# Optimization experiments

Measured on AMD Instinct MI355X. Metric: run time of the kernel, lower is better.

The kernel has to match this reference:

```python
import jax, jax.numpy as jnp
import numpy as np

D = 768
H = 12
DH = D // H
DFF = 4 * D
B, S = 2, 2048


def setup_inputs() -> dict:
    key = jax.random.key(0)
    ks = jax.random.split(key, 12)
    inp = {
        "X": jax.random.normal(ks[0], (B, S, D), dtype=jnp.float32),
        # per-head projections, stacked over heads (nn.Linear: y = x W^T + b; we store W already transposed as [d, d_h])
        "Wq": jax.random.normal(ks[1], (H, D, DH), dtype=jnp.float32) * (1.0 / np.sqrt(D)),
        "bq": jnp.zeros((H, DH), dtype=jnp.float32),
        "Wk": jax.random.normal(ks[2], (H, D, DH), dtype=jnp.float32) * (1.0 / np.sqrt(D)),
        "bk": jnp.zeros((H, DH), dtype=jnp.float32),
        "Wv": jax.random.normal(ks[3], (H, D, DH), dtype=jnp.float32) * (1.0 / np.sqrt(D)),
        "bv": jnp.zeros((H, DH), dtype=jnp.float32),
        "W0": jax.random.normal(ks[4], (D, D), dtype=jnp.float32) * (1.0 / np.sqrt(D)),
        "b0": jnp.zeros((D,), dtype=jnp.float32),
        # FFN params are torch.randn (unit std) in the original
        "W1": jax.random.normal(ks[5], (D, DFF), dtype=jnp.float32),
        "b1": jnp.zeros((DFF,), dtype=jnp.float32),
        "W2": jax.random.normal(ks[6], (DFF, D), dtype=jnp.float32),
        "b2": jnp.zeros((D,), dtype=jnp.float32),
        "g1": jnp.ones((D,), dtype=jnp.float32),
        "o1": jnp.zeros((D,), dtype=jnp.float32),
        "g2": jnp.ones((D,), dtype=jnp.float32),
        "o2": jnp.zeros((D,), dtype=jnp.float32),
    }
    return inp


def _layernorm(x, gain, offset):
    # original: (x - mean) / (std + 1e-5)  with population std (unbiased=False)
    m = jnp.mean(x, axis=-1, keepdims=True)
    sd = jnp.sqrt(jnp.mean((x - m) ** 2, axis=-1, keepdims=True))
    return gain * ((x - m) / (sd + 1e-5)) + offset


def _mha(x, Wq, bq, Wk, bk, Wv, bv, W0, b0):
    # batched over heads; equivalent to the per-head SHA loop + concat
    q = jnp.einsum("bsd,hdk->bhsk", x, Wq) + bq[None, :, None, :]
    k = jnp.einsum("bsd,hdk->bhsk", x, Wk) + bk[None, :, None, :]
    v = jnp.einsum("bsd,hdk->bhsk", x, Wv) + bv[None, :, None, :]
    scores = jnp.einsum("bhsk,bhtk->bhst", q, k) / np.sqrt(DH).astype(np.float32)
    seq = x.shape[1]
    causal = jnp.tril(jnp.ones((seq, seq), dtype=bool))
    scores = jnp.where(causal[None, None], scores, -jnp.inf)
    w = jax.nn.softmax(scores, axis=-1)
    out = jnp.einsum("bhst,bhtk->bhsk", w, v)
    out = jnp.transpose(out, (0, 2, 1, 3)).reshape(x.shape[0], seq, D)  # concat heads
    return out @ W0 + b0


def reference(X, Wq, bq, Wk, bk, Wv, bv, W0, b0, W1, b1, W2, b2, g1, o1, g2, o2):
    h = X + _mha(_layernorm(X, g1, o1), Wq, bq, Wk, bk, Wv, bv, W0, b0)
    y = _layernorm(h, g2, o2)
    y = jnp.maximum(y @ W1 + b1, 0.0) @ W2 + b2
    return h + y
```

## Files before the change

kernel.cpp:

```cpp
#include <hip/hip_runtime.h>
#include <hip/hip_bf16.h>
#include <cstdint>

#define BB 2
#define SS 2048
#define DD 768
#define HH 12
#define DHH 64
#define DFF 3072
#define MM (BB * SS)

typedef __attribute__((ext_vector_type(8))) short bf16x8;
typedef __attribute__((ext_vector_type(4))) float f32x4;
typedef __attribute__((ext_vector_type(16))) float f32x16;
typedef __attribute__((ext_vector_type(4))) unsigned short u16x4;
typedef __attribute__((ext_vector_type(8))) unsigned short u16x8;
typedef unsigned int u32;

#define DEV static __device__ __forceinline__

typedef __attribute__((address_space(1))) void AS1void;
typedef __attribute__((address_space(3))) void AS3void;

DEV void async_copy16(const void* g, void* l) {
  __builtin_amdgcn_global_load_lds((AS1void*)g, (AS3void*)l, 16, 0, 0);
}

DEV unsigned short bf16bits(float f) {
  __hip_bfloat16 h = __float2bfloat16(f);
  return *(unsigned short*)&h;
}

DEV u32 pack2(float a, float b) {
  return ((u32)bf16bits(b) << 16) | (u32)bf16bits(a);
}

__global__ __launch_bounds__(256) void ln_kernel(
    const float* __restrict__ x, const float* __restrict__ gain,
    const float* __restrict__ off, __hip_bfloat16* __restrict__ out)
{
  const int wave = threadIdx.x >> 6;
  const int lane = threadIdx.x & 63;
  const int row = blockIdx.x * 4 + wave;
  const float* xr = x + (size_t)row * DD;

  float4 v[3];
  float s1 = 0.f, s2 = 0.f;
#pragma unroll
  for (int j = 0; j < 3; ++j) {
    v[j] = *(const float4*)(xr + (j * 64 + lane) * 4);
    s1 += v[j].x + v[j].y + v[j].z + v[j].w;
    s2 += v[j].x * v[j].x + v[j].y * v[j].y + v[j].z * v[j].z + v[j].w * v[j].w;
  }
#pragma unroll
  for (int d = 1; d < 64; d <<= 1) {
    s1 += __shfl_xor(s1, d);
    s2 += __shfl_xor(s2, d);
  }
  const float mean = s1 * (1.0f / 768.0f);
  const float var = fmaxf(s2 * (1.0f / 768.0f) - mean * mean, 0.0f);
  const float rs = 1.0f / (sqrtf(var) + 1e-5f);

  unsigned short* orow = (unsigned short*)out + (size_t)row * DD;
#pragma unroll
  for (int j = 0; j < 3; ++j) {
    const int c = (j * 64 + lane) * 4;
    float4 g4 = *(const float4*)(gain + c);
    float4 o4 = *(const float4*)(off + c);
    u16x4 pk;
    pk[0] = bf16bits(g4.x * ((v[j].x - mean) * rs) + o4.x);
    pk[1] = bf16bits(g4.y * ((v[j].y - mean) * rs) + o4.y);
    pk[2] = bf16bits(g4.z * ((v[j].z - mean) * rs) + o4.z);
    pk[3] = bf16bits(g4.w * ((v[j].w - mean) * rs) + o4.w);
    *(u16x4*)(orow + c) = pk;
  }
}

__global__ __launch_bounds__(256) void transpose_generic(
    const float* __restrict__ in, __hip_bfloat16* __restrict__ out, int R, int C)
{
  __shared__ float tile[64][65];
  const int c0 = blockIdx.x * 64, r0 = blockIdx.y * 64;
  for (int i = threadIdx.x; i < 4096; i += 256) {
    int r = i >> 6, c = i & 63;
    tile[r][c] = in[(size_t)(r0 + r) * C + c0 + c];
  }
  __syncthreads();
  for (int i = threadIdx.x; i < 4096; i += 256) {
    int c = i >> 6, r = i & 63;
    out[(size_t)(c0 + c) * R + r0 + r] = __float2bfloat16(tile[r][c]);
  }
}

__global__ __launch_bounds__(256) void transpose_qkv(
    const float* __restrict__ Wq, const float* __restrict__ Wk,
    const float* __restrict__ Wv, __hip_bfloat16* __restrict__ out)
{
  __shared__ float tile[64][65];
  const int z = blockIdx.z;
  const int p = z / HH, h = z - p * HH;
  const float* in = (p == 0 ? Wq : (p == 1 ? Wk : Wv)) + (size_t)h * DD * DHH;
  const int r0 = blockIdx.y * 64;
  for (int i = threadIdx.x; i < 4096; i += 256) {
    int r = i >> 6, c = i & 63;
    tile[r][c] = in[(size_t)(r0 + r) * DHH + c];
  }
  __syncthreads();
  for (int i = threadIdx.x; i < 4096; i += 256) {
    int c = i >> 6, r = i & 63;
    out[(size_t)(p * DD + h * DHH + c) * DD + r0 + r] = __float2bfloat16(tile[r][c]);
  }
}

__global__ __launch_bounds__(256) void kvimg_kernel(
    const __hip_bfloat16* __restrict__ qkv, char* __restrict__ kimg,
    char* __restrict__ vimg)
{
  __shared__ unsigned short tileK[64][72];
  __shared__ unsigned short tileV[64][72];
  const int bh = blockIdx.y;
  const int b = bh / HH, h = bh - (bh / HH) * HH;
  const int t0 = blockIdx.x * 64;
  const int HD = 3 * DD;
  const unsigned short* Kp = (const unsigned short*)qkv + (size_t)(b * SS) * HD + DD + h * DHH;
  const unsigned short* Vp = (const unsigned short*)qkv + (size_t)(b * SS) * HD + 2 * DD + h * DHH;
  char* kdst = kimg + ((size_t)bh * 32 + blockIdx.x) * 8192;
  char* vdst = vimg + ((size_t)bh * 32 + blockIdx.x) * 8192;

  for (int i = threadIdx.x; i < 512; i += 256) {
    const int r = i >> 3, c8 = (i & 7) * 8;
    *(bf16x8*)&tileK[r][c8] = *(const bf16x8*)(Kp + (size_t)(t0 + r) * HD + c8);
    *(bf16x8*)&tileV[r][c8] = *(const bf16x8*)(Vp + (size_t)(t0 + r) * HD + c8);
  }
  __syncthreads();
  for (int i = threadIdx.x; i < 512; i += 256) {
    const int f = i >> 6, l = i & 63;
    const int kc = f >> 1, half = f & 1;
    const int lc = l & 31, lh = l >> 5;
    *(bf16x8*)(kdst + i * 16) = *(const bf16x8*)&tileK[half * 32 + lc][kc * 16 + lh * 8];
    union { unsigned short u[8]; bf16x8 v; } w;
#pragma unroll
    for (int e = 0; e < 8; ++e) w.u[e] = tileV[kc * 16 + lh * 8 + e][half * 32 + lc];
    *(bf16x8*)(vdst + i * 16) = w.v;
  }
}

template<bool RELU, bool OUT_BF16, bool HAS_RES>
__global__ __launch_bounds__(256) void gemm_bt(
    const __hip_bfloat16* __restrict__ A, const __hip_bfloat16* __restrict__ BT,
    const float* __restrict__ bias, const float* __restrict__ res,
    void* __restrict__ outp, int M, int N, int K)
{
  __shared__ __hip_bfloat16 Alds[2][128 * 32];
  __shared__ __hip_bfloat16 Blds[2][128 * 32];
  const int tid = threadIdx.x;
  const int wave = tid >> 6;
  const int lane = tid & 63;
  const int fr = lane & 15, fq = lane >> 4;
  const int wr = wave >> 1, wc = wave & 1;
  const int bm = blockIdx.y * 128, bn = blockIdx.x * 128;

  const int srow = tid >> 2;
  const int scol = (tid & 3) * 8;
  const __hip_bfloat16* ag0 = A + (size_t)(bm + srow) * K + scol;
  const __hip_bfloat16* ag1 = A + (size_t)(bm + 64 + srow) * K + scol;
  const __hip_bfloat16* bg0 = BT + (size_t)(bn + srow) * K + scol;
  const __hip_bfloat16* bg1 = BT + (size_t)(bn + 64 + srow) * K + scol;
  const int so = wave * 512;

  f32x4 acc[4][4] = {};

  async_copy16(ag0, &Alds[0][so]);
  async_copy16(ag1, &Alds[0][2048 + so]);
  async_copy16(bg0, &Blds[0][so]);
  async_copy16(bg1, &Blds[0][2048 + so]);
  __syncthreads();

  const int niter = K / 32;
  for (int i = 0; i < niter; ++i) {
    const int cur = i & 1;
    if (i + 1 < niter) {
      const int k1 = (i + 1) * 32;
      async_copy16(ag0 + k1, &Alds[cur ^ 1][so]);
      async_copy16(ag1 + k1, &Alds[cur ^ 1][2048 + so]);
      async_copy16(bg0 + k1, &Blds[cur ^ 1][so]);
      async_copy16(bg1 + k1, &Blds[cur ^ 1][2048 + so]);
    }
    bf16x8 af[4], bfr[4];
#pragma unroll
    for (int i4 = 0; i4 < 4; ++i4)
      af[i4] = *(const bf16x8*)(&Alds[cur][(wr * 64 + i4 * 16 + fr) * 32 + fq * 8]);
#pragma unroll
    for (int j4 = 0; j4 < 4; ++j4)
      bfr[j4] = *(const bf16x8*)(&Blds[cur][(wc * 64 + j4 * 16 + fr) * 32 + fq * 8]);
#pragma unroll
    for (int i4 = 0; i4 < 4; ++i4)
#pragma unroll
      for (int j4 = 0; j4 < 4; ++j4)
        acc[i4][j4] = __builtin_amdgcn_mfma_f32_16x16x32_bf16(af[i4], bfr[j4], acc[i4][j4], 0, 0, 0);
    __syncthreads();
  }

#pragma unroll
  for (int j = 0; j < 4; ++j) {
    const int c = bn + wc * 64 + j * 16 + fr;
    const float bv = bias[c];
#pragma unroll
    for (int i = 0; i < 4; ++i) {
#pragma unroll
      for (int r = 0; r < 4; ++r) {
        const int rr = bm + wr * 64 + i * 16 + fq * 4 + r;
        float v = acc[i][j][r] + bv;
        if (RELU) v = fmaxf(v, 0.0f);
        if (HAS_RES) v += res[(size_t)rr * N + c];
        if (OUT_BF16) ((__hip_bfloat16*)outp)[(size_t)rr * N + c] = __float2bfloat16(v);
        else          ((float*)outp)[(size_t)rr * N + c] = v;
      }
    }
  }
}

__global__ __launch_bounds__(256) void gemm_bt_sk(
    const __hip_bfloat16* __restrict__ A, const __hip_bfloat16* __restrict__ BT,
    float* __restrict__ part01, float* __restrict__ part23,
    int M, int N, int K, int K_per)
{
  __shared__ __hip_bfloat16 Alds[2][128 * 32];
  __shared__ __hip_bfloat16 Blds[2][128 * 32];
  const int tid = threadIdx.x;
  const int wave = tid >> 6;
  const int lane = tid & 63;
  const int fr = lane & 15, fq = lane >> 4;
  const int wr = wave >> 1, wc = wave & 1;
  const int bm = blockIdx.y * 128, bn = blockIdx.x * 128;
  const int z = blockIdx.z;
  float* part = (z < 2 ? part01 : part23) + (size_t)(z & 1) * M * N;
  const int kbase = z * K_per;

  const int srow = tid >> 2;
  const int scol = (tid & 3) * 8;
  const __hip_bfloat16* ag0 = A + (size_t)(bm + srow) * K + scol + kbase;
  const __hip_bfloat16* ag1 = A + (size_t)(bm + 64 + srow) * K + scol + kbase;
  const __hip_bfloat16* bg0 = BT + (size_t)(bn + srow) * K + scol + kbase;
  const __hip_bfloat16* bg1 = BT + (size_t)(bn + 64 + srow) * K + scol + kbase;
  const int so = wave * 512;

  f32x4 acc[4][4] = {};

  async_copy16(ag0, &Alds[0][so]);
  async_copy16(ag1, &Alds[0][2048 + so]);
  async_copy16(bg0, &Blds[0][so]);
  async_copy16(bg1, &Blds[0][2048 + so]);
  __syncthreads();

  const int niter = K_per / 32;
  for (int i = 0; i < niter; ++i) {
    const int cur = i & 1;
    if (i + 1 < niter) {
      const int k1 = (i + 1) * 32;
      async_copy16(ag0 + k1, &Alds[cur ^ 1][so]);
      async_copy16(ag1 + k1, &Alds[cur ^ 1][2048 + so]);
      async_copy16(bg0 + k1, &Blds[cur ^ 1][so]);
      async_copy16(bg1 + k1, &Blds[cur ^ 1][2048 + so]);
    }
    bf16x8 af[4], bfr[4];
#pragma unroll
    for (int i4 = 0; i4 < 4; ++i4)
      af[i4] = *(const bf16x8*)(&Alds[cur][(wr * 64 + i4 * 16 + fr) * 32 + fq * 8]);
#pragma unroll
    for (int j4 = 0; j4 < 4; ++j4)
      bfr[j4] = *(const bf16x8*)(&Blds[cur][(wc * 64 + j4 * 16 + fr) * 32 + fq * 8]);
#pragma unroll
    for (int i4 = 0; i4 < 4; ++i4)
#pragma unroll
      for (int j4 = 0; j4 < 4; ++j4)
        acc[i4][j4] = __builtin_amdgcn_mfma_f32_16x16x32_bf16(af[i4], bfr[j4], acc[i4][j4], 0, 0, 0);
    __syncthreads();
  }

#pragma unroll
  for (int j = 0; j < 4; ++j) {
    const int c = bn + wc * 64 + j * 16 + fr;
#pragma unroll
    for (int i = 0; i < 4; ++i) {
#pragma unroll
      for (int r = 0; r < 4; ++r) {
        const int rr = bm + wr * 64 + i * 16 + fq * 4 + r;
        part[(size_t)rr * N + c] = acc[i][j][r];
      }
    }
  }
}

__global__ __launch_bounds__(256) void combine4(
    const float* __restrict__ part01, const float* __restrict__ part23,
    const float* __restrict__ res, const float* __restrict__ bias,
    float* __restrict__ out, int MN, int N)
{
  const int idx = (blockIdx.x * 256 + threadIdx.x) * 4;
  if (idx >= MN) return;
  const float4 a0 = *(const float4*)(part01 + idx);
  const float4 a1 = *(const float4*)(part01 + MN + idx);
  const float4 a2 = *(const float4*)(part23 + idx);
  const float4 a3 = *(const float4*)(part23 + MN + idx);
  const float4 rr = *(const float4*)(res + idx);
  const float4 bb = *(const float4*)(bias + (idx % N));
  float4 o;
  o.x = a0.x + a1.x + a2.x + a3.x + rr.x + bb.x;
  o.y = a0.y + a1.y + a2.y + a3.y + rr.y + bb.y;
  o.z = a0.z + a1.z + a2.z + a3.z + rr.z + bb.z;
  o.w = a0.w + a1.w + a2.w + a3.w + rr.w + bb.w;
  *(float4*)(out + idx) = o;
}

__global__ __launch_bounds__(128, 3) void attn_kernel(
    const __hip_bfloat16* __restrict__ qkv, const char* __restrict__ kimg,
    const char* __restrict__ vimg, __hip_bfloat16* __restrict__ outp)
{
  const int HD = 3 * DD;
  const int id = blockIdx.x;
  const int xcd = id & 7;
  const int j = id >> 3;
  const int s2 = 63 - j / 3;
  const int bhl = j - 3 * (j / 3);
  const int bh = xcd * 3 + bhl;
  const int b = bh / HH, h = bh - (bh / HH) * HH;

  const int q0w = s2 * 32;
  const int tid = threadIdx.x;
  const int c = tid >> 6;
  const int lane = tid & 63;
  const int col = lane & 31, hi = lane >> 5;
  const int qg = q0w + col;

  const size_t base = (size_t)b * SS * HD;
  const __hip_bfloat16* Qp = qkv + base + h * DHH;
  const char* kimg_h = kimg + (size_t)bh * 32 * 8192;
  const char* vimg_h = vimg + (size_t)bh * 32 * 8192;

  __shared__ __align__(16) char sm[17408];

  bf16x8 qf[4];
#pragma unroll
  for (int kc = 0; kc < 4; ++kc)
    qf[kc] = *(const bf16x8*)(Qp + (size_t)qg * HD + kc * 16 + hi * 8);

  f32x16 o0 = {}, o1 = {};
  float mreg = -1e30f, lreg = 0.f;
  const float CS = 0.125f * 1.44269504f;

  const int ntiles = (q0w >> 6) + 1;

  bf16x8 kf[8];
  {
    const char* ks = kimg_h + (size_t)c * 8192 + lane * 16;
#pragma unroll
    for (int f = 0; f < 8; ++f) kf[f] = *(const bf16x8*)(ks + f * 1024);
  }

  for (int t = c; t < ntiles; t += 2) {
    const int kv0 = t * 64;
    f32x16 s0 = {}, s1 = {};
    __builtin_amdgcn_s_setprio(1);
#pragma unroll
    for (int kc = 0; kc < 4; ++kc) {
      s0 = __builtin_amdgcn_mfma_f32_32x32x16_bf16(kf[kc * 2],     qf[kc], s0, 0, 0, 0);
      s1 = __builtin_amdgcn_mfma_f32_32x32x16_bf16(kf[kc * 2 + 1], qf[kc], s1, 0, 0, 0);
    }
    __builtin_amdgcn_s_setprio(0);
    bf16x8 vf[8];
    {
      const char* vs = vimg_h + (size_t)t * 8192 + lane * 16;
#pragma unroll
      for (int f = 0; f < 8; ++f) vf[f] = *(const bf16x8*)(vs + f * 1024);
    }
    if (t + 2 < ntiles) {
      const char* ks = kimg_h + (size_t)(t + 2) * 8192 + lane * 16;
#pragma unroll
      for (int f = 0; f < 8; ++f) kf[f] = *(const bf16x8*)(ks + f * 1024);
    }
    if (kv0 + 63 > q0w) {
#pragma unroll
      for (int r = 0; r < 16; ++r) {
        const int tl = (r & 3) + 8 * (r >> 2) + 4 * hi;
        s0[r] = (kv0 + tl <= qg) ? s0[r] : -1e30f;
        s1[r] = (kv0 + 32 + tl <= qg) ? s1[r] : -1e30f;
      }
    }
    float mx = s0[0];
#pragma unroll
    for (int r = 1; r < 16; ++r) mx = fmaxf(mx, s0[r]);
#pragma unroll
    for (int r = 0; r < 16; ++r) mx = fmaxf(mx, s1[r]);
    mx = fmaxf(mx, __shfl_xor(mx, 32));
    const float mnew = fmaxf(mreg, mx);
    const float alpha = exp2f((mreg - mnew) * CS);
    mreg = mnew;
    const float mc = mnew * CS;
    float ps = 0.f;
#pragma unroll
    for (int r = 0; r < 16; ++r) {
      const float p0 = exp2f(s0[r] * CS - mc); s0[r] = p0; ps += p0;
      const float p1 = exp2f(s1[r] * CS - mc); s1[r] = p1; ps += p1;
    }
    ps += __shfl_xor(ps, 32);
    lreg = lreg * alpha + ps;
#pragma unroll
    for (int r = 0; r < 16; ++r) { o0[r] *= alpha; o1[r] *= alpha; }

    u32 pk0[4][2], pk1[4][2];
#pragma unroll
    for (int qd = 0; qd < 4; ++qd) {
      pk0[qd][0] = pack2(s0[4 * qd + 0], s0[4 * qd + 1]);
      pk0[qd][1] = pack2(s0[4 * qd + 2], s0[4 * qd + 3]);
      pk1[qd][0] = pack2(s1[4 * qd + 0], s1[4 * qd + 1]);
      pk1[qd][1] = pack2(s1[4 * qd + 2], s1[4 * qd + 3]);
    }
#pragma unroll
    for (int kc = 0; kc < 4; ++kc) {
      const int qa = 2 * (kc & 1), qb = qa + 1;
      const u32 A0 = (kc < 2) ? pk0[qa][0] : pk1[qa][0];
      const u32 A1 = (kc < 2) ? pk0[qa][1] : pk1[qa][1];
      const u32 B0 = (kc < 2) ? pk0[qb][0] : pk1[qb][0];
      const u32 B1 = (kc < 2) ? pk0[qb][1] : pk1[qb][1];
      const u32 send0 = hi ? A0 : B0;
      const u32 send1 = hi ? A1 : B1;
      const u32 recv0 = __shfl_xor(send0, 32);
      const u32 recv1 = __shfl_xor(send1, 32);
      const u32 su0 = hi ? B0 : A0;
      const u32 su1 = hi ? B1 : A1;
      union { u32 u[4]; bf16x8 v; } pf;
      pf.u[0] = hi ? recv0 : su0;
      pf.u[1] = hi ? recv1 : su1;
      pf.u[2] = hi ? su0 : recv0;
      pf.u[3] = hi ? su1 : recv1;
      __builtin_amdgcn_s_setprio(1);
      o0 = __builtin_amdgcn_mfma_f32_32x32x16_bf16(vf[kc * 2],     pf.v, o0, 0, 0, 0);
      o1 = __builtin_amdgcn_mfma_f32_32x32x16_bf16(vf[kc * 2 + 1], pf.v, o1, 0, 0, 0);
      __builtin_amdgcn_s_setprio(0);
    }
  }

  float* opart = (float*)sm;
  float* mlp   = (float*)(sm + 16640);
#pragma unroll
  for (int r = 0; r < 16; ++r) {
    const int d = (r & 3) + 8 * (r >> 2) + 4 * hi;
    opart[(c * 32 + col) * 65 + d]      = o0[r];
    opart[(c * 32 + col) * 65 + d + 32] = o1[r];
  }
  if (hi == 0) {
    mlp[c * 64 + col]      = mreg;
    mlp[c * 64 + 32 + col] = lreg;
  }
  __syncthreads();

  const int q = tid >> 2;
  const int d0 = (tid & 3) * 16;
  float mcv[2], lcv[2];
#pragma unroll
  for (int cc = 0; cc < 2; ++cc) {
    mcv[cc] = mlp[cc * 64 + q];
    lcv[cc] = mlp[cc * 64 + 32 + q];
  }
  const float mstar = fmaxf(mcv[0], mcv[1]);
  float av[2], lstar = 0.f;
#pragma unroll
  for (int cc = 0; cc < 2; ++cc) {
    av[cc] = exp2f((mcv[cc] - mstar) * CS);
    lstar += av[cc] * lcv[cc];
  }
  const float inv = 1.0f / lstar;
  float acc[16] = {};
#pragma unroll
  for (int cc = 0; cc < 2; ++cc) {
    const float a = av[cc];
#pragma unroll
    for (int e = 0; e < 16; ++e)
      acc[e] += a * opart[(cc * 32 + q) * 65 + d0 + e];
  }
  unsigned short* orow = (unsigned short*)outp +
      (size_t)(b * SS + q0w + q) * DD + h * DHH + d0;
  u16x8 w8;
#pragma unroll
  for (int e = 0; e < 8; ++e) w8[e] = bf16bits(acc[e] * inv);
  *(u16x8*)orow = w8;
#pragma unroll
  for (int e = 0; e < 8; ++e) w8[e] = bf16bits(acc[8 + e] * inv);
  *(u16x8*)(orow + 8) = w8;
}

extern "C" void kernel_launch(void* const* d_in, const int* in_sizes, int n_in,
                              void* d_out, int out_size, void* d_ws, size_t ws_size,
                              hipStream_t stream)
{
  (void)in_sizes; (void)n_in; (void)out_size; (void)ws_size;
  const float* X  = (const float*)d_in[0];
  const float* Wq = (const float*)d_in[1];
  const float* bq = (const float*)d_in[2];
  const float* Wk = (const float*)d_in[3];
  const float* bk = (const float*)d_in[4];
  const float* Wv = (const float*)d_in[5];
  const float* bv = (const float*)d_in[6];
  const float* W0 = (const float*)d_in[7];
  const float* b0 = (const float*)d_in[8];
  const float* W1 = (const float*)d_in[9];
  const float* b1 = (const float*)d_in[10];
  const float* W2 = (const float*)d_in[11];
  const float* b2 = (const float*)d_in[12];
  const float* g1 = (const float*)d_in[13];
  const float* o1 = (const float*)d_in[14];
  const float* g2 = (const float*)d_in[15];
  const float* o2 = (const float*)d_in[16];

  char* ws = (char*)d_ws;
  auto alloc = [&](size_t bytes) {
    char* p = ws;
    ws += (bytes + 255) & ~(size_t)255;
    return p;
  };
  __hip_bfloat16* ln1    = (__hip_bfloat16*)alloc((size_t)MM * DD * 2);
  __hip_bfloat16* qkvb16 = (__hip_bfloat16*)alloc((size_t)MM * 3 * DD * 2);
  __hip_bfloat16* attnb  = (__hip_bfloat16*)alloc((size_t)MM * DD * 2);
  float*          hbuf   = (float*)alloc((size_t)MM * DD * 4);
  __hip_bfloat16* ln2    = (__hip_bfloat16*)alloc((size_t)MM * DD * 2);
  __hip_bfloat16* ffn1   = (__hip_bfloat16*)alloc((size_t)MM * DFF * 2);
  __hip_bfloat16* WqkvT  = (__hip_bfloat16*)alloc((size_t)3 * DD * DD * 2);
  __hip_bfloat16* W0T    = (__hip_bfloat16*)alloc((size_t)DD * DD * 2);
  __hip_bfloat16* W1T    = (__hip_bfloat16*)alloc((size_t)DFF * DD * 2);
  __hip_bfloat16* W2T    = (__hip_bfloat16*)alloc((size_t)DD * DFF * 2);
  float*          qkvbias= (float*)alloc((size_t)3 * DD * 4);
  float*          part23 = (float*)alloc((size_t)2 * MM * DD * 4);
  char*           kimg   = alloc((size_t)24 * 32 * 8192);
  char*           vimg   = alloc((size_t)24 * 32 * 8192);
  float*          part01 = (float*)ln1;

  transpose_qkv<<<dim3(1, 12, 36), 256, 0, stream>>>(Wq, Wk, Wv, WqkvT);
  transpose_generic<<<dim3(12, 12), 256, 0, stream>>>(W0, W0T, DD, DD);
  transpose_generic<<<dim3(48, 12), 256, 0, stream>>>(W1, W1T, DD, DFF);
  transpose_generic<<<dim3(12, 48), 256, 0, stream>>>(W2, W2T, DFF, DD);
  hipMemcpyAsync(qkvbias,          bq, DD * 4, hipMemcpyDeviceToDevice, stream);
  hipMemcpyAsync(qkvbias + DD,     bk, DD * 4, hipMemcpyDeviceToDevice, stream);
  hipMemcpyAsync(qkvbias + 2 * DD, bv, DD * 4, hipMemcpyDeviceToDevice, stream);

  ln_kernel<<<MM / 4, 256, 0, stream>>>(X, g1, o1, ln1);
  gemm_bt<false, true, false><<<dim3(3 * DD / 128, MM / 128), 256, 0, stream>>>(
      ln1, WqkvT, qkvbias, nullptr, qkvb16, MM, 3 * DD, DD);
  kvimg_kernel<<<dim3(SS / 64, BB * HH), 256, 0, stream>>>(qkvb16, kimg, vimg);
  attn_kernel<<<1536, 128, 0, stream>>>(qkvb16, kimg, vimg, attnb);
  gemm_bt<false, false, true><<<dim3(DD / 128, MM / 128), 256, 0, stream>>>(
      attnb, W0T, b0, X, hbuf, MM, DD, DD);
  ln_kernel<<<MM / 4, 256, 0, stream>>>(hbuf, g2, o2, ln2);
  gemm_bt<true, true, false><<<dim3(DFF / 128, MM / 128), 256, 0, stream>>>(
      ln2, W1T, b1, nullptr, ffn1, MM, DFF, DD);
  gemm_bt_sk<<<dim3(DD / 128, MM / 128, 4), 256, 0, stream>>>(
      ffn1, W2T, part01, part23, MM, DD, DFF, DFF / 4);
  combine4<<<(MM * DD) / 1024, 256, 0, stream>>>(
      part01, part23, hbuf, b2, (float*)d_out, MM * DD, DD);
}
```

Before: 206.7 us.

## Store split-K partials in bf16 and hoist V fragment loads before QK MFMAs

The split-K FFN2 GEMM now writes its four partial sums as bf16 instead of fp32, and the combine kernel widens them back to fp32 before adding them. This halves the partial-sum write and read traffic, at the cost of extra rounding error in the output. The partials are large because W2 has unit std, so absolute error grows. Separately, the attention kernel issues its V-tile loads before the QK MFMAs so that their latency overlaps with compute. This raises register pressure.

```diff
diff --git a/kernel.cpp b/kernel.cpp
--- a/kernel.cpp
+++ b/kernel.cpp
@@ -29,6 +29,12 @@
 DEV unsigned short bf16bits(float f) {
   __hip_bfloat16 h = __float2bfloat16(f);
   return *(unsigned short*)&h;
+}
+
+DEV float bits2f(unsigned short u) {
+  u32 x = ((u32)u) << 16;
+  union { u32 u; float f; } c; c.u = x;
+  return c.f;
 }
 
 DEV u32 pack2(float a, float b) {
@@ -222,7 +228,7 @@
 
 __global__ __launch_bounds__(256) void gemm_bt_sk(
     const __hip_bfloat16* __restrict__ A, const __hip_bfloat16* __restrict__ BT,
-    float* __restrict__ part01, float* __restrict__ part23,
+    unsigned short* __restrict__ part01, unsigned short* __restrict__ part23,
     int M, int N, int K, int K_per)
 {
   __shared__ __hip_bfloat16 Alds[2][128 * 32];
@@ -234,7 +240,7 @@
   const int wr = wave >> 1, wc = wave & 1;
   const int bm = blockIdx.y * 128, bn = blockIdx.x * 128;
   const int z = blockIdx.z;
-  float* part = (z < 2 ? part01 : part23) + (size_t)(z & 1) * M * N;
+  unsigned short* part = (z < 2 ? part01 : part23) + (size_t)(z & 1) * M * N;
   const int kbase = z * K_per;
 
   const int srow = tid >> 2;
@@ -286,30 +292,30 @@
 #pragma unroll
       for (int r = 0; r < 4; ++r) {
         const int rr = bm + wr * 64 + i * 16 + fq * 4 + r;
-        part[(size_t)rr * N + c] = acc[i][j][r];
+        part[(size_t)rr * N + c] = bf16bits(acc[i][j][r]);
       }
     }
   }
 }
 
 __global__ __launch_bounds__(256) void combine4(
-    const float* __restrict__ part01, const float* __restrict__ part23,
+    const unsigned short* __restrict__ part01, const unsigned short* __restrict__ part23,
     const float* __restrict__ res, const float* __restrict__ bias,
     float* __restrict__ out, int MN, int N)
 {
   const int idx = (blockIdx.x * 256 + threadIdx.x) * 4;
   if (idx >= MN) return;
-  const float4 a0 = *(const float4*)(part01 + idx);
-  const float4 a1 = *(const float4*)(part01 + MN + idx);
-  const float4 a2 = *(const float4*)(part23 + idx);
-  const float4 a3 = *(const float4*)(part23 + MN + idx);
+  const u16x4 a0 = *(const u16x4*)(part01 + idx);
+  const u16x4 a1 = *(const u16x4*)(part01 + MN + idx);
+  const u16x4 a2 = *(const u16x4*)(part23 + idx);
+  const u16x4 a3 = *(const u16x4*)(part23 + MN + idx);
   const float4 rr = *(const float4*)(res + idx);
   const float4 bb = *(const float4*)(bias + (idx % N));
   float4 o;
-  o.x = a0.x + a1.x + a2.x + a3.x + rr.x + bb.x;
-  o.y = a0.y + a1.y + a2.y + a3.y + rr.y + bb.y;
-  o.z = a0.z + a1.z + a2.z + a3.z + rr.z + bb.z;
-  o.w = a0.w + a1.w + a2.w + a3.w + rr.w + bb.w;
+  o.x = bits2f(a0[0]) + bits2f(a1[0]) + bits2f(a2[0]) + bits2f(a3[0]) + rr.x + bb.x;
+  o.y = bits2f(a0[1]) + bits2f(a1[1]) + bits2f(a2[1]) + bits2f(a3[1]) + rr.y + bb.y;
+  o.z = bits2f(a0[2]) + bits2f(a1[2]) + bits2f(a2[2]) + bits2f(a3[2]) + rr.z + bb.z;
+  o.w = bits2f(a0[3]) + bits2f(a1[3]) + bits2f(a2[3]) + bits2f(a3[3]) + rr.w + bb.w;
   *(float4*)(out + idx) = o;
 }
 
@@ -360,6 +366,12 @@
 
   for (int t = c; t < ntiles; t += 2) {
     const int kv0 = t * 64;
+    bf16x8 vf[8];
+    {
+      const char* vs = vimg_h + (size_t)t * 8192 + lane * 16;
+#pragma unroll
+      for (int f = 0; f < 8; ++f) vf[f] = *(const bf16x8*)(vs + f * 1024);
+    }
     f32x16 s0 = {}, s1 = {};
     __builtin_amdgcn_s_setprio(1);
 #pragma unroll
@@ -368,12 +380,6 @@
       s1 = __builtin_amdgcn_mfma_f32_32x32x16_bf16(kf[kc * 2 + 1], qf[kc], s1, 0, 0, 0);
     }
     __builtin_amdgcn_s_setprio(0);
-    bf16x8 vf[8];
-    {
-      const char* vs = vimg_h + (size_t)t * 8192 + lane * 16;
-#pragma unroll
-      for (int f = 0; f < 8; ++f) vf[f] = *(const bf16x8*)(vs + f * 1024);
-    }
     if (t + 2 < ntiles) {
       const char* ks = kimg_h + (size_t)(t + 2) * 8192 + lane * 16;
 #pragma unroll
@@ -530,10 +536,10 @@
   __hip_bfloat16* W1T    = (__hip_bfloat16*)alloc((size_t)DFF * DD * 2);
   __hip_bfloat16* W2T    = (__hip_bfloat16*)alloc((size_t)DD * DFF * 2);
   float*          qkvbias= (float*)alloc((size_t)3 * DD * 4);
-  float*          part23 = (float*)alloc((size_t)2 * MM * DD * 4);
+  unsigned short* part23 = (unsigned short*)alloc((size_t)2 * MM * DD * 2);
   char*           kimg   = alloc((size_t)24 * 32 * 8192);
   char*           vimg   = alloc((size_t)24 * 32 * 8192);
-  float*          part01 = (float*)ln1;
+  unsigned short* part01 = (unsigned short*)ln1;
 
   transpose_qkv<<<dim3(1, 12, 36), 256, 0, stream>>>(Wq, Wk, Wv, WqkvT);
   transpose_generic<<<dim3(12, 12), 256, 0, stream>>>(W0, W0T, DD, DD);
```

Result: faster. 201.0 us (-2.8%).
